# Kernel tuning notes

Hardware: AMD Instinct MI355X
Metric: run time of the kernel (lower is better)

## Reference

```python
import jax, jax.numpy as jnp
import numpy as np

N = 8192
IN_F = 128
OUT_F = 128


def setup_inputs() -> dict:
    key = jax.random.key(0)
    k1, k2, k3, k4 = jax.random.split(key, 4)
    h = jax.random.normal(k1, (N, IN_F), dtype=jnp.float32)
    pos = jax.random.normal(k2, (N, 1, 3), dtype=jnp.float32)
    # xavier_uniform-ish scale for params
    W = jax.random.uniform(k3, (IN_F, OUT_F), dtype=jnp.float32,
                           minval=-1.0, maxval=1.0) * (1.414 * np.sqrt(6.0 / (IN_F + OUT_F)))
    a = jax.random.uniform(k4, (2 * OUT_F + 3, 1), dtype=jnp.float32,
                           minval=-1.0, maxval=1.0) * (1.414 * np.sqrt(6.0 / (2 * OUT_F + 3 + 1)))
    return {"h": h, "pos": pos, "W": W, "a": a}


def reference(h, pos, W, a):
    # Wh: [N, F]
    Wh = h @ W
    F_ = Wh.shape[1]
    a1 = a[:F_, 0]          # weights on Wh[j] (the repeated / neighbor features)
    a2 = a[F_:2 * F_, 0]    # weights on Wh[i] (the repeat_interleaved / center features)
    a3 = a[2 * F_:, 0]      # weights on pos[i] - pos[j]
    p = pos.reshape(-1, 3)  # [N, 3]
    s_j = Wh @ a1           # [N]
    s_i = Wh @ a2           # [N]
    p_a = p @ a3            # [N]
    # e[i, j] = leaky_relu(Wh[j].a1 + Wh[i].a2 + (pos[i]-pos[j]).a3)
    e = jax.nn.leaky_relu(s_i[:, None] + s_j[None, :] + p_a[:, None] - p_a[None, :],
                          negative_slope=0.2)  # [N, N]
    attention = jax.nn.softmax(e, axis=1)
    # eval mode: dropout is identity
    h_prime = attention @ Wh  # [N, F]
    return jax.nn.elu(h_prime)
```

## Files before the change

### kernel.cpp

```cpp
#include <hip/hip_runtime.h>
#include <hip/hip_bf16.h>

#define N 8192
#define F 128
#define JC 16
#define JSLICE (N / JC)

typedef __attribute__((ext_vector_type(4)))  float f32x4;
typedef __attribute__((ext_vector_type(16))) float f32x16;
typedef __attribute__((ext_vector_type(8)))  short short8;

static __device__ __forceinline__ short bf16bits(float x) {
  __hip_bfloat16 b = __float2bfloat16(x);
  return *reinterpret_cast<short*>(&b);
}

__global__ __launch_bounds__(256) void k_gemm_cd(
    const float* __restrict__ h, const float* __restrict__ pos,
    const float* __restrict__ W, const float* __restrict__ a,
    unsigned short* __restrict__ WhTf, float* __restrict__ cArr,
    float* __restrict__ dArr)
{
  __shared__ float Ws[128 * 128];
  const int tid = threadIdx.x;
  const int r0  = blockIdx.x * 16;

  {
    f32x4* Ws4 = (f32x4*)Ws;
    const f32x4* Wg4 = (const f32x4*)W;
#pragma unroll
    for (int q = 0; q < 16; ++q) Ws4[q * 256 + tid] = Wg4[q * 256 + tid];
  }
  __syncthreads();

  const int rg  = tid >> 5;
  const int c32 = tid & 31;

  f32x4 acc0, acc1;
#pragma unroll
  for (int i = 0; i < 4; ++i) { acc0[i] = 0.0f; acc1[i] = 0.0f; }

  const f32x4* h40 = (const f32x4*)(h + (size_t)(r0 + rg * 2) * 128);
  const f32x4* h41 = (const f32x4*)(h + (size_t)(r0 + rg * 2 + 1) * 128);
  const f32x4* Ws4 = (const f32x4*)Ws;

#pragma unroll 4
  for (int k4 = 0; k4 < 32; ++k4) {
    f32x4 hv0 = h40[k4];
    f32x4 hv1 = h41[k4];
#pragma unroll
    for (int e = 0; e < 4; ++e) {
      f32x4 w = Ws4[(k4 * 4 + e) * 32 + c32];
      acc0 += hv0[e] * w;
      acc1 += hv1[e] * w;
    }
  }

  f32x4 a1v = *(const f32x4*)(a + c32 * 4);
  f32x4 a2v = *(const f32x4*)(a + 128 + c32 * 4);
#pragma unroll
  for (int rr = 0; rr < 2; ++rr) {
    f32x4 accR = rr ? acc1 : acc0;
    f32x4 t1 = accR * a1v;
    f32x4 t2 = accR * a2v;
    float s1 = t1[0] + t1[1] + t1[2] + t1[3];
    float s2 = t2[0] + t2[1] + t2[2] + t2[3];
#pragma unroll
    for (int m = 1; m < 32; m <<= 1) {
      s1 += __shfl_xor(s1, m);
      s2 += __shfl_xor(s2, m);
    }
    if (c32 == 0) {
      const int row = r0 + rg * 2 + rr;
      float pa = pos[row * 3 + 0] * a[256] + pos[row * 3 + 1] * a[257] +
                 pos[row * 3 + 2] * a[258];
      cArr[row] = s2 + pa;
      dArr[row] = s1 - pa;
    }
  }

  __syncthreads();
  float* tmp = Ws;
  {
    const int base = (rg * 2) * 132 + c32 * 4;
    *(f32x4*)&tmp[base]       = acc0;
    *(f32x4*)&tmp[base + 132] = acc1;
  }
  __syncthreads();
  {
    const int col  = tid >> 1;
    const int half = tid & 1;
    short8 o;
#pragma unroll
    for (int rr = 0; rr < 8; ++rr)
      o[rr] = bf16bits(tmp[(half * 8 + rr) * 132 + col]);
    *(short8*)(WhTf + (size_t)(r0 >> 4) * 2048 + col * 16 + half * 8) = o;
  }
}

__global__ __launch_bounds__(256, 4) void k_flash(
    const unsigned short* __restrict__ WhTf, const float* __restrict__ cArr,
    const float* __restrict__ dArr, float* __restrict__ pnum,
    float* __restrict__ pden)
{
  __shared__ __align__(16) float dS[JSLICE];

  const int tid = threadIdx.x;
  const int rb  = blockIdx.x & 63;
  const int jc  = blockIdx.x >> 6;
  const int r0  = rb * 128;

  const int w  = tid >> 6;
  const int l  = tid & 63;
  const int cl = l & 31;
  const int kh = l >> 5;

  if (tid < JSLICE / 4)
    ((f32x4*)dS)[tid] = ((const f32x4*)(dArr + (size_t)jc * JSLICE))[tid];
  __syncthreads();

  const float L2E = 1.44269504f;
  const float ci = cArr[r0 + w * 32 + cl] * L2E;

  f32x16 acc0, acc1, acc2, acc3;
#pragma unroll
  for (int i = 0; i < 16; ++i) { acc0[i] = 0; acc1[i] = 0; acc2[i] = 0; acc3[i] = 0; }
  float denA = 0.0f, denB = 0.0f;

  const unsigned short* bPtr =
      WhTf + (size_t)(jc * (JSLICE / 16)) * 2048 + cl * 16 + kh * 8;
  const float* dPtr = dS + kh * 8;

  short8 b0 = *(const short8*)(bPtr);
  short8 b1 = *(const short8*)(bPtr + 512);
  short8 b2 = *(const short8*)(bPtr + 1024);
  short8 b3 = *(const short8*)(bPtr + 1536);
  bPtr += 2048;

  const int iters = JSLICE / 16;
  for (int s = 0; s < iters; ++s) {
    short8 n0 = *(const short8*)(bPtr);
    short8 n1 = *(const short8*)(bPtr + 512);
    short8 n2 = *(const short8*)(bPtr + 1024);
    short8 n3 = *(const short8*)(bPtr + 1536);

    f32x4 dj0 = *(const f32x4*)(dPtr);
    f32x4 dj1 = *(const f32x4*)(dPtr + 4);

    short8 af;
#pragma unroll
    for (int e = 0; e < 8; ++e) {
      float dj = (e < 4) ? dj0[e] : dj1[e - 4];
      float u = __builtin_fmaf(dj, L2E, ci);
      u = fmaxf(u, 0.2f * u);
      float pv = __builtin_amdgcn_exp2f(u);
      if (e & 1) denB += pv; else denA += pv;
      af[e] = bf16bits(pv);
    }

    acc0 = __builtin_amdgcn_mfma_f32_32x32x16_bf16(af, b0, acc0, 0, 0, 0);
    acc1 = __builtin_amdgcn_mfma_f32_32x32x16_bf16(af, b1, acc1, 0, 0, 0);
    acc2 = __builtin_amdgcn_mfma_f32_32x32x16_bf16(af, b2, acc2, 0, 0, 0);
    acc3 = __builtin_amdgcn_mfma_f32_32x32x16_bf16(af, b3, acc3, 0, 0, 0);

    b0 = n0; b1 = n1; b2 = n2; b3 = n3;
    bPtr += 2048; dPtr += 16;
  }

  float den = denA + denB;
  den += __shfl_xor(den, 32);

  {
    float* base = pnum + (size_t)jc * N * F + (size_t)(r0 + w * 32) * 128;
#pragma unroll
    for (int reg = 0; reg < 16; ++reg) {
      const int row = (reg & 3) + 8 * (reg >> 2) + 4 * kh;
      float* rp = base + row * 128 + cl;
      rp[0]  = acc0[reg];
      rp[32] = acc1[reg];
      rp[64] = acc2[reg];
      rp[96] = acc3[reg];
    }
    if (l < 32) pden[(size_t)jc * N + r0 + w * 32 + l] = den;
  }
}

__global__ __launch_bounds__(256) void k_final(
    const float* __restrict__ pnum, const float* __restrict__ pden,
    float* __restrict__ out)
{
  const int g = blockIdx.x * 256 + threadIdx.x;
  const int row = g >> 5;
  f32x4 n;
#pragma unroll
  for (int i = 0; i < 4; ++i) n[i] = 0.0f;
  float dd = 0.0f;
#pragma unroll
  for (int c = 0; c < JC; ++c) {
    n += ((const f32x4*)pnum)[(size_t)c * (N * F / 4) + g];
    dd += pden[(size_t)c * N + row];
  }
  f32x4 r = n * (1.0f / dd);
#pragma unroll
  for (int i = 0; i < 4; ++i) {
    float x = r[i];
    r[i] = x > 0.0f ? x : (__builtin_amdgcn_exp2f(x * 1.44269504f) - 1.0f);
  }
  ((f32x4*)out)[g] = r;
}

extern "C" void kernel_launch(void* const* d_in, const int* in_sizes, int n_in,
                              void* d_out, int out_size, void* d_ws, size_t ws_size,
                              hipStream_t stream)
{
  const float* h   = (const float*)d_in[0];
  const float* pos = (const float*)d_in[1];
  const float* W   = (const float*)d_in[2];
  const float* a   = (const float*)d_in[3];
  float* out = (float*)d_out;

  char* ws = (char*)d_ws;
  unsigned short* WhTf = (unsigned short*)ws;
  float* cArr = (float*)(ws + (size_t)2 * 1024 * 1024);
  float* dArr = cArr + N;
  float* pden = dArr + N;
  float* pnum = pden + (size_t)JC * N;

  hipLaunchKernelGGL(k_gemm_cd, dim3(512), dim3(256), 0, stream,
                     h, pos, W, a, WhTf, cArr, dArr);
  hipLaunchKernelGGL(k_flash, dim3(64 * JC), dim3(256), 0, stream,
                     WhTf, cArr, dArr, pnum, pden);
  hipLaunchKernelGGL(k_final, dim3((N * F / 4) / 256), dim3(256), 0, stream,
                     pnum, pden, out);
}
```

Baseline: 111.2 us.

## Replace dense attention with sort-based prefix/suffix sums exploiting separable logits

Because the attention logit is c_i + d_j and leaky_relu is piecewise linear, exp factors into per-row and per-column terms on each side of the breakpoint. The code sorts d by rank counting, builds prefix sums of exp(0.2 d)·Wh and suffix sums of exp(d)·Wh in a chunked two-pass scan, then binary-searches each row's breakpoint to assemble the softmax output. This removes the O(N²) exp and MFMA work in exchange for several small, serial, low-parallelism kernels and unnormalized exponentials that could lose precision or overflow for large logits.

Result: slower. 145.1 us (+30.4%).

```diff
diff --git a/kernel.cpp b/kernel.cpp
--- a/kernel.cpp
+++ b/kernel.cpp
@@ -3,23 +3,15 @@
 
 #define N 8192
 #define F 128
-#define JC 16
-#define JSLICE (N / JC)
-
-typedef __attribute__((ext_vector_type(4)))  float f32x4;
-typedef __attribute__((ext_vector_type(16))) float f32x16;
-typedef __attribute__((ext_vector_type(8)))  short short8;
-
-static __device__ __forceinline__ short bf16bits(float x) {
-  __hip_bfloat16 b = __float2bfloat16(x);
-  return *reinterpret_cast<short*>(&b);
-}
-
-__global__ __launch_bounds__(256) void k_gemm_cd(
+#define L2E 1.44269504f
+
+typedef __attribute__((ext_vector_type(4))) float f32x4;
+typedef __attribute__((ext_vector_type(4))) unsigned int u32x4;
+
+__global__ __launch_bounds__(256) void k_wh(
     const float* __restrict__ h, const float* __restrict__ pos,
     const float* __restrict__ W, const float* __restrict__ a,
-    unsigned short* __restrict__ WhTf, float* __restrict__ cArr,
-    float* __restrict__ dArr)
+    float* __restrict__ Wh, float* __restrict__ cArr, float* __restrict__ dArr)
 {
   __shared__ float Ws[128 * 128];
   const int tid = threadIdx.x;
@@ -54,6 +46,12 @@
       acc0 += hv0[e] * w;
       acc1 += hv1[e] * w;
     }
+  }
+
+  {
+    float* wp = Wh + (size_t)(r0 + rg * 2) * 128 + c32 * 4;
+    *(f32x4*)wp         = acc0;
+    *(f32x4*)(wp + 128) = acc1;
   }
 
   f32x4 a1v = *(const f32x4*)(a + c32 * 4);
@@ -78,135 +76,178 @@
       dArr[row] = s1 - pa;
     }
   }
-
-  __syncthreads();
-  float* tmp = Ws;
-  {
-    const int base = (rg * 2) * 132 + c32 * 4;
-    *(f32x4*)&tmp[base]       = acc0;
-    *(f32x4*)&tmp[base + 132] = acc1;
-  }
-  __syncthreads();
-  {
-    const int col  = tid >> 1;
-    const int half = tid & 1;
-    short8 o;
-#pragma unroll
-    for (int rr = 0; rr < 8; ++rr)
-      o[rr] = bf16bits(tmp[(half * 8 + rr) * 132 + col]);
-    *(short8*)(WhTf + (size_t)(r0 >> 4) * 2048 + col * 16 + half * 8) = o;
-  }
-}
-
-__global__ __launch_bounds__(256, 4) void k_flash(
-    const unsigned short* __restrict__ WhTf, const float* __restrict__ cArr,
-    const float* __restrict__ dArr, float* __restrict__ pnum,
-    float* __restrict__ pden)
-{
-  __shared__ __align__(16) float dS[JSLICE];
-
+}
+
+__global__ __launch_bounds__(512) void k_rank(
+    const float* __restrict__ dArr, float* __restrict__ sortedD,
+    int* __restrict__ perm)
+{
+  __shared__ unsigned int keyS[N];
   const int tid = threadIdx.x;
-  const int rb  = blockIdx.x & 63;
-  const int jc  = blockIdx.x >> 6;
-  const int r0  = rb * 128;
-
-  const int w  = tid >> 6;
-  const int l  = tid & 63;
-  const int cl = l & 31;
-  const int kh = l >> 5;
-
-  if (tid < JSLICE / 4)
-    ((f32x4*)dS)[tid] = ((const f32x4*)(dArr + (size_t)jc * JSLICE))[tid];
-  __syncthreads();
-
-  const float L2E = 1.44269504f;
-  const float ci = cArr[r0 + w * 32 + cl] * L2E;
-
-  f32x16 acc0, acc1, acc2, acc3;
-#pragma unroll
-  for (int i = 0; i < 16; ++i) { acc0[i] = 0; acc1[i] = 0; acc2[i] = 0; acc3[i] = 0; }
-  float denA = 0.0f, denB = 0.0f;
-
-  const unsigned short* bPtr =
-      WhTf + (size_t)(jc * (JSLICE / 16)) * 2048 + cl * 16 + kh * 8;
-  const float* dPtr = dS + kh * 8;
-
-  short8 b0 = *(const short8*)(bPtr);
-  short8 b1 = *(const short8*)(bPtr + 512);
-  short8 b2 = *(const short8*)(bPtr + 1024);
-  short8 b3 = *(const short8*)(bPtr + 1536);
-  bPtr += 2048;
-
-  const int iters = JSLICE / 16;
-  for (int s = 0; s < iters; ++s) {
-    short8 n0 = *(const short8*)(bPtr);
-    short8 n1 = *(const short8*)(bPtr + 512);
-    short8 n2 = *(const short8*)(bPtr + 1024);
-    short8 n3 = *(const short8*)(bPtr + 1536);
-
-    f32x4 dj0 = *(const f32x4*)(dPtr);
-    f32x4 dj1 = *(const f32x4*)(dPtr + 4);
-
-    short8 af;
-#pragma unroll
-    for (int e = 0; e < 8; ++e) {
-      float dj = (e < 4) ? dj0[e] : dj1[e - 4];
-      float u = __builtin_fmaf(dj, L2E, ci);
-      u = fmaxf(u, 0.2f * u);
-      float pv = __builtin_amdgcn_exp2f(u);
-      if (e & 1) denB += pv; else denA += pv;
-      af[e] = bf16bits(pv);
-    }
-
-    acc0 = __builtin_amdgcn_mfma_f32_32x32x16_bf16(af, b0, acc0, 0, 0, 0);
-    acc1 = __builtin_amdgcn_mfma_f32_32x32x16_bf16(af, b1, acc1, 0, 0, 0);
-    acc2 = __builtin_amdgcn_mfma_f32_32x32x16_bf16(af, b2, acc2, 0, 0, 0);
-    acc3 = __builtin_amdgcn_mfma_f32_32x32x16_bf16(af, b3, acc3, 0, 0, 0);
-
-    b0 = n0; b1 = n1; b2 = n2; b3 = n3;
-    bPtr += 2048; dPtr += 16;
-  }
-
-  float den = denA + denB;
-  den += __shfl_xor(den, 32);
-
-  {
-    float* base = pnum + (size_t)jc * N * F + (size_t)(r0 + w * 32) * 128;
-#pragma unroll
-    for (int reg = 0; reg < 16; ++reg) {
-      const int row = (reg & 3) + 8 * (reg >> 2) + 4 * kh;
-      float* rp = base + row * 128 + cl;
-      rp[0]  = acc0[reg];
-      rp[32] = acc1[reg];
-      rp[64] = acc2[reg];
-      rp[96] = acc3[reg];
-    }
-    if (l < 32) pden[(size_t)jc * N + r0 + w * 32 + l] = den;
-  }
-}
-
-__global__ __launch_bounds__(256) void k_final(
-    const float* __restrict__ pnum, const float* __restrict__ pden,
+
+#pragma unroll
+  for (int q = 0; q < 4; ++q) {
+    int i4 = q * 512 + tid;
+    f32x4 v = ((const f32x4*)dArr)[i4];
+    u32x4 kk;
+#pragma unroll
+    for (int e = 0; e < 4; ++e) {
+      union { float f; unsigned u; } cv; cv.f = v[e];
+      kk[e] = (cv.u >> 31) ? ~cv.u : (cv.u | 0x80000000u);
+    }
+    ((u32x4*)keyS)[i4] = kk;
+  }
+  __syncthreads();
+
+  const int g = tid >> 4;
+  const int L = tid & 15;
+  const int j = blockIdx.x * 32 + g;
+  const unsigned int myk = keyS[j];
+
+  int cnt = 0;
+#pragma unroll 4
+  for (int it = 0; it < 128; ++it) {
+    const int u = it * 16 + L;
+    u32x4 kv = ((const u32x4*)keyS)[u];
+    const int p = u * 4;
+#pragma unroll
+    for (int e = 0; e < 4; ++e)
+      cnt += (kv[e] < myk) || (kv[e] == myk && (p + e) < j);
+  }
+#pragma unroll
+  for (int m = 1; m < 16; m <<= 1) cnt += __shfl_xor(cnt, m);
+
+  if (L == 0) {
+    sortedD[cnt] = dArr[j];
+    perm[cnt] = j;
+  }
+}
+
+__global__ __launch_bounds__(256) void k_scan(
+    const float* __restrict__ Wh, const float* __restrict__ sortedD,
+    const int* __restrict__ perm, float* __restrict__ chunkTot)
+{
+  __shared__ float sA[128], sB[128], sdA[2], sdB[2];
+  const int tid  = threadIdx.x;
+  const int f    = tid & 127;
+  const int half = tid >> 7;
+  const int base = blockIdx.x * 128 + half * 64;
+
+  float tA = 0, tB = 0, dA = 0, dB = 0;
+#pragma unroll 4
+  for (int m = 0; m < 64; ++m) {
+    float d = sortedD[base + m];
+    int row = perm[base + m];
+    float w1 = __builtin_amdgcn_exp2f(0.2f * L2E * d);
+    float w2 = __builtin_amdgcn_exp2f(L2E * d);
+    float v  = Wh[(size_t)row * 128 + f];
+    tA += w1 * v; tB += w2 * v; dA += w1; dB += w2;
+  }
+  if (half == 1) {
+    sA[f] = tA; sB[f] = tB;
+    if (f == 0) { sdA[1] = dA; sdB[1] = dB; }
+  }
+  __syncthreads();
+  if (half == 0) {
+    float* ct = chunkTot + blockIdx.x * 260;
+    ct[f]       = tA + sA[f];
+    ct[128 + f] = tB + sB[f];
+    if (f == 0) { ct[256] = dA + sdA[1]; ct[257] = dB + sdB[1]; }
+  }
+}
+
+__global__ __launch_bounds__(256) void k_emit(
+    const float* __restrict__ Wh, const float* __restrict__ sortedD,
+    const int* __restrict__ perm, const float* __restrict__ chunkTot,
+    float* __restrict__ Apre, float* __restrict__ Bsuf,
+    float* __restrict__ denPre, float* __restrict__ denSuf)
+{
+  const int tid  = threadIdx.x;
+  const int f    = tid & 127;
+  const int half = tid >> 7;
+  const int c    = blockIdx.x;
+  const int base = c * 128;
+
+  if (half == 0) {
+    float off = 0, offd = 0;
+    for (int cc = 0; cc < c; ++cc) {
+      off  += chunkTot[cc * 260 + f];
+      offd += chunkTot[cc * 260 + 256];
+    }
+    if (c == 0) { Apre[f] = 0.0f; if (f == 0) denPre[0] = 0.0f; }
+    float Arun = off, dArun = offd;
+#pragma unroll 2
+    for (int m = 0; m < 128; ++m) {
+      float d = sortedD[base + m];
+      int row = perm[base + m];
+      float v = Wh[(size_t)row * 128 + f];
+      float w1 = __builtin_amdgcn_exp2f(0.2f * L2E * d);
+      Arun += w1 * v; dArun += w1;
+      Apre[(size_t)(base + m + 1) * 128 + f] = Arun;
+      if (f == 0) denPre[base + m + 1] = dArun;
+    }
+  } else {
+    float off = 0, offd = 0;
+    for (int cc = c + 1; cc < 64; ++cc) {
+      off  += chunkTot[cc * 260 + 128 + f];
+      offd += chunkTot[cc * 260 + 257];
+    }
+    if (c == 63) { Bsuf[(size_t)N * 128 + f] = 0.0f; if (f == 0) denSuf[N] = 0.0f; }
+    float Brun = off, dBrun = offd;
+#pragma unroll 2
+    for (int m = 127; m >= 0; --m) {
+      float d = sortedD[base + m];
+      int row = perm[base + m];
+      float v = Wh[(size_t)row * 128 + f];
+      float w2 = __builtin_amdgcn_exp2f(L2E * d);
+      Brun += w2 * v; dBrun += w2;
+      Bsuf[(size_t)(base + m) * 128 + f] = Brun;
+      if (f == 0) denSuf[base + m] = dBrun;
+    }
+  }
+}
+
+__global__ __launch_bounds__(256) void k_out(
+    const float* __restrict__ cArr, const float* __restrict__ sortedD,
+    const float* __restrict__ Apre, const float* __restrict__ Bsuf,
+    const float* __restrict__ denPre, const float* __restrict__ denSuf,
     float* __restrict__ out)
 {
-  const int g = blockIdx.x * 256 + threadIdx.x;
-  const int row = g >> 5;
-  f32x4 n;
-#pragma unroll
-  for (int i = 0; i < 4; ++i) n[i] = 0.0f;
-  float dd = 0.0f;
-#pragma unroll
-  for (int c = 0; c < JC; ++c) {
-    n += ((const f32x4*)pnum)[(size_t)c * (N * F / 4) + g];
-    dd += pden[(size_t)c * N + row];
-  }
-  f32x4 r = n * (1.0f / dd);
-#pragma unroll
-  for (int i = 0; i < 4; ++i) {
-    float x = r[i];
-    r[i] = x > 0.0f ? x : (__builtin_amdgcn_exp2f(x * 1.44269504f) - 1.0f);
-  }
-  ((f32x4*)out)[g] = r;
+  __shared__ float sd[N];
+  const int tid = threadIdx.x;
+#pragma unroll
+  for (int q = 0; q < 8; ++q)
+    ((f32x4*)sd)[q * 256 + tid] = ((const f32x4*)sortedD)[q * 256 + tid];
+  __syncthreads();
+
+  const int grp = tid >> 5;
+  const int cl  = tid & 31;
+#pragma unroll
+  for (int pass = 0; pass < 8; ++pass) {
+    const int r = blockIdx.x * 64 + pass * 8 + grp;
+    const float c = cArr[r];
+    const float t = -c;
+    int lo = 0, hi = N;
+#pragma unroll
+    for (int it = 0; it < 13; ++it) {
+      int mid = (lo + hi) >> 1;
+      if (sd[mid] <= t) lo = mid + 1; else hi = mid;
+    }
+    const int k = lo;
+    const float e2 = __builtin_amdgcn_exp2f(0.2f * L2E * c);
+    const float e1 = __builtin_amdgcn_exp2f(L2E * c);
+    f32x4 A4 = *(const f32x4*)(Apre + (size_t)k * 128 + cl * 4);
+    f32x4 B4 = *(const f32x4*)(Bsuf + (size_t)k * 128 + cl * 4);
+    const float den = e2 * denPre[k] + e1 * denSuf[k];
+    const float inv = 1.0f / den;
+    f32x4 o;
+#pragma unroll
+    for (int i = 0; i < 4; ++i) {
+      float x = (e2 * A4[i] + e1 * B4[i]) * inv;
+      o[i] = x > 0.0f ? x : (__builtin_amdgcn_exp2f(x * L2E) - 1.0f);
+    }
+    *(f32x4*)(out + (size_t)r * 128 + cl * 4) = o;
+  }
 }
 
 extern "C" void kernel_launch(void* const* d_in, const int* in_sizes, int n_in,
@@ -219,17 +260,27 @@
   const float* a   = (const float*)d_in[3];
   float* out = (float*)d_out;
 
-  char* ws = (char*)d_ws;
-  unsigned short* WhTf = (unsigned short*)ws;
-  float* cArr = (float*)(ws + (size_t)2 * 1024 * 1024);
-  float* dArr = cArr + N;
-  float* pden = dArr + N;
-  float* pnum = pden + (size_t)JC * N;
-
-  hipLaunchKernelGGL(k_gemm_cd, dim3(512), dim3(256), 0, stream,
-                     h, pos, W, a, WhTf, cArr, dArr);
-  hipLaunchKernelGGL(k_flash, dim3(64 * JC), dim3(256), 0, stream,
-                     WhTf, cArr, dArr, pnum, pden);
-  hipLaunchKernelGGL(k_final, dim3((N * F / 4) / 256), dim3(256), 0, stream,
-                     pnum, pden, out);
-}
+  float* ws = (float*)d_ws;
+  size_t off = 0;
+  float* Wh      = ws + off; off += (size_t)N * F;
+  float* cArr    = ws + off; off += N;
+  float* dArr    = ws + off; off += N;
+  float* sortedD = ws + off; off += N;
+  int*   perm    = (int*)(ws + off); off += N;
+  float* denPre  = ws + off; off += N + 8;
+  float* denSuf  = ws + off; off += N + 8;
+  float* chunkTot= ws + off; off += 64 * 260;
+  float* Apre    = ws + off; off += (size_t)(N + 1) * F + 32;
+  float* Bsuf    = ws + off; off += (size_t)(N + 1) * F + 32;
+
+  hipLaunchKernelGGL(k_wh,   dim3(512), dim3(256), 0, stream,
+                     h, pos, W, a, Wh, cArr, dArr);
+  hipLaunchKernelGGL(k_rank, dim3(256), dim3(512), 0, stream,
+                     dArr, sortedD, perm);
+  hipLaunchKernelGGL(k_scan, dim3(64), dim3(256), 0, stream,
+                     Wh, sortedD, perm, chunkTot);
+  hipLaunchKernelGGL(k_emit, dim3(64), dim3(256), 0, stream,
+                     Wh, sortedD, perm, chunkTot, Apre, Bsuf, denPre, denSuf);
+  hipLaunchKernelGGL(k_out,  dim3(128), dim3(256), 0, stream,
+                     cArr, sortedD, Apre, Bsuf, denPre, denSuf, out);
+}
```
